# Performance work log

Hardware: AMD Instinct MI355X
Metric: run time of the kernel (lower is better)

The kernel has to match this reference:

```python
import jax, jax.numpy as jnp
import numpy as np

EPS = 1e-06  # used both as eps and as the F.threshold threshold (mqjs passes eps as th)


def _pair_log_dist_sum(x1, x2, th):
    # dist[i,j] = ||x1_i||^2 + ||x2_j||^2 - 2 x1_i . x2_j  (n x n)
    x1x2 = x1 @ x2.T
    sq1 = jnp.sum(x1 * x1, axis=1)[:, None]
    sq2 = jnp.sum(x2 * x2, axis=1)[None, :]
    dist = sq1 + sq2 - 2.0 * x1x2
    # F.threshold(dist, th, 1): values <= th -> 1; then clamp(min=1), sqrt, log, row-sum
    dist = jnp.where(dist > th, dist, 1.0)
    dist = jnp.maximum(dist, 1.0)
    return jnp.sum(0.5 * jnp.log(dist), axis=1)  # log(sqrt(d)) == 0.5*log(d)


def _mqjs(inp, tgt, eps):
    n = inp.shape[0]
    x1 = inp.reshape(n, -1)
    x2 = tgt.reshape(n, -1)
    p = (x1 + x2) / 2.0
    ce = _pair_log_dist_sum(x1, p, eps) + _pair_log_dist_sum(x2, p, eps)
    se = _pair_log_dist_sum(x1, x1, eps) * (n / (n - 1))
    return jnp.mean(ce - se)


def setup_inputs() -> dict:
    key = jax.random.key(0)
    k1, k2 = jax.random.split(key)
    n, d = 8192, 256
    inp = jax.random.normal(k1, (n, d), dtype=jnp.float32)
    tgt = jax.random.normal(k2, (n, d), dtype=jnp.float32)
    return {"input": inp, "target": tgt}


def reference(input, target):
    return _mqjs(input, target, EPS)
```

## Files before the change

kernel.cpp:

```cpp
#include <hip/hip_runtime.h>

#define N 8192
#define D 256
#define BM 128
#define BJ 64
#define JG 8
#define GJ (N / BJ / JG)
#define GI (N / BM)
#define NPART (3 * GI * GJ)

typedef int   i32x4 __attribute__((ext_vector_type(4)));
typedef int   i32x8 __attribute__((ext_vector_type(8)));
typedef float f32x4 __attribute__((ext_vector_type(4)));
typedef float f32x2 __attribute__((ext_vector_type(2)));

__device__ __forceinline__ unsigned pack_fp8x4(float a, float b, float c, float d) {
    unsigned lo = __builtin_amdgcn_cvt_pk_fp8_f32(a, b, 0, false);
    return __builtin_amdgcn_cvt_pk_fp8_f32(c, d, lo, true);
}
__device__ __forceinline__ float dequant_sumsq(unsigned q) {
    const float v0 = __builtin_amdgcn_cvt_f32_fp8(q, 0);
    const float v1 = __builtin_amdgcn_cvt_f32_fp8(q, 1);
    const float v2 = __builtin_amdgcn_cvt_f32_fp8(q, 2);
    const float v3 = __builtin_amdgcn_cvt_f32_fp8(q, 3);
    return fmaf(v0, v0, fmaf(v1, v1, fmaf(v2, v2, v3 * v3)));
}

__global__ void prep_kernel(const float* __restrict__ x1, const float* __restrict__ x2,
                            unsigned* __restrict__ x1q, unsigned* __restrict__ x2q,
                            unsigned* __restrict__ pq,
                            float* __restrict__ sq1, float* __restrict__ sq2,
                            float* __restrict__ sqp) {
    const int tid = threadIdx.x, lane = tid & 63, wv = tid >> 6;
    const int row = blockIdx.x * 4 + wv;
    const size_t eb = (size_t)row * D + lane * 4;
    const float4 a = *(const float4*)(x1 + eb);
    const float4 b = *(const float4*)(x2 + eb);
    const float px = 0.5f * (a.x + b.x), py = 0.5f * (a.y + b.y);
    const float pz = 0.5f * (a.z + b.z), pw = 0.5f * (a.w + b.w);
    const unsigned qa = pack_fp8x4(a.x, a.y, a.z, a.w);
    const unsigned qb = pack_fp8x4(b.x, b.y, b.z, b.w);
    const unsigned qp = pack_fp8x4(px, py, pz, pw);
    const size_t wb = (size_t)row * (D / 4) + lane;
    x1q[wb] = qa; x2q[wb] = qb; pq[wb] = qp;
    float s1 = dequant_sumsq(qa), s2 = dequant_sumsq(qb), sp = dequant_sumsq(qp);
    #pragma unroll
    for (int o = 32; o > 0; o >>= 1) {
        s1 += __shfl_down(s1, o, 64);
        s2 += __shfl_down(s2, o, 64);
        sp += __shfl_down(sp, o, 64);
    }
    if (lane == 0) { sq1[row] = s1; sq2[row] = s2; sqp[row] = sp; }
}

__device__ __forceinline__ f32x4 mfma8(i32x8 a, i32x8 b, f32x4 c) {
    return __builtin_amdgcn_mfma_scale_f32_16x16x128_f8f6f4(
        a, b, c, 0, 0, 0, 0x7F7F7F7F, 0, 0x7F7F7F7F);
}

__device__ __forceinline__ i32x8 read_frag(const unsigned char* Ts, int m, int quad) {
    const int r7 = m & 7;
    const i32x4 lo = *(const i32x4*)(Ts + m * 128 + ((((2 * quad)     ^ r7)) << 4));
    const i32x4 hi = *(const i32x4*)(Ts + m * 128 + ((((2 * quad + 1) ^ r7)) << 4));
    i32x8 f;
    f[0] = lo[0]; f[1] = lo[1]; f[2] = lo[2]; f[3] = lo[3];
    f[4] = hi[0]; f[5] = hi[1]; f[6] = hi[2]; f[7] = hi[3];
    return f;
}

__device__ __forceinline__ void stageB(const unsigned char* __restrict__ g,
                                       unsigned char* s, int rowbase, size_t kb,
                                       int wv, int srow, int sblk) {
    #pragma unroll
    for (int it = 0; it < 2; ++it) {
        const int grp = wv * 2 + it;
        const int row = grp * 8 + srow;
        __builtin_amdgcn_global_load_lds(
            (const __attribute__((address_space(1))) void*)(g + (size_t)(rowbase + row) * D + kb + sblk * 16),
            (__attribute__((address_space(3))) void*)(s + grp * 1024), 16, 0, 0);
    }
}

__device__ __forceinline__ float logsumP(const f32x4 (&acc)[4][2],
                                         const f32x2 (&sa01)[4], const f32x2 (&sa23)[4],
                                         const float sb[2]) {
    float s = 0.0f;
    #pragma unroll
    for (int ti = 0; ti < 4; ++ti) {
        f32x2 pr = {1.0f, 1.0f};
        #pragma unroll
        for (int tj = 0; tj < 2; ++tj) {
            const f32x2 sbv = {sb[tj], sb[tj]};
            const f32x2 t01 = sa01[ti] + sbv, t23 = sa23[ti] + sbv;
            const f32x2 v01 = {acc[ti][tj][0], acc[ti][tj][1]};
            const f32x2 v23 = {acc[ti][tj][2], acc[ti][tj][3]};
            f32x2 d01 = t01 - 2.0f * v01;
            f32x2 d23 = t23 - 2.0f * v23;
            d01 = __builtin_elementwise_max(d01, (f32x2){1.0f, 1.0f});
            d23 = __builtin_elementwise_max(d23, (f32x2){1.0f, 1.0f});
            pr *= d01; pr *= d23;
        }
        s += __logf(pr.x * pr.y);
    }
    return s;
}

__device__ __forceinline__ float logsumStraddle(const f32x4 (&acc)[4][2],
                                                const f32x2 (&sa01)[4], const f32x2 (&sa23)[4],
                                                const float sb[2],
                                                int wr, int wc, int quad, int l15,
                                                int I0, int J0) {
    float s = 0.0f;
    #pragma unroll
    for (int ti = 0; ti < 4; ++ti) {
        #pragma unroll
        for (int tj = 0; tj < 2; ++tj) {
            const int j = J0 + wc * 32 + tj * 16 + l15;
            float pr = 1.0f;
            #pragma unroll
            for (int r = 0; r < 4; ++r) {
                const int i = I0 + wr * 64 + ti * 16 + quad * 4 + r;
                const float sav = (r < 2) ? ((r & 1) ? sa01[ti].y : sa01[ti].x)
                                          : ((r & 1) ? sa23[ti].y : sa23[ti].x);
                float d = fmaf(-2.0f, acc[ti][tj][r], sav + sb[tj]);
                d = fmaxf(d, 1.0f);
                const float t = (j > i) ? d : 1.0f;
                const float u = (j >= i) ? d : 1.0f;
                pr *= t * u;
            }
            s += __logf(pr);
        }
    }
    return s;
}

__global__ __launch_bounds__(256) void mqjs_main(
    const unsigned char* __restrict__ x1q, const unsigned char* __restrict__ x2q,
    const unsigned char* __restrict__ pq,
    const float* __restrict__ sq1, const float* __restrict__ sq2,
    const float* __restrict__ sqp, float* __restrict__ partials) {

    __shared__ __align__(16) unsigned char Bs[2][2 * BJ * 128];
    __shared__ float red[4];

    const int tid = threadIdx.x;
    const int lane = tid & 63;
    const int wv = tid >> 6;
    const int wr = wv >> 1, wc = wv & 1;
    const int quad = lane >> 4, l15 = lane & 15;
    const int srow = lane >> 3;
    const int sblk = (lane & 7) ^ srow;

    const int z = blockIdx.z;
    const int I0 = blockIdx.y * BM;
    const int jbase = blockIdx.x * JG;
    const int pid = (z * GI + blockIdx.y) * GJ + blockIdx.x;
    const float wse = -(float)N / (float)(N - 1);

    int jj0 = 0;
    if (z == 2) {
        jj0 = 2 * (int)blockIdx.y - jbase;
        if (jj0 < 0) jj0 = 0;
        if (jj0 >= JG) { if (tid == 0) partials[pid] = 0.0f; return; }
    }

    const unsigned char* Ag = (z == 1) ? x2q : x1q;
    const unsigned char* Bg = (z == 2) ? x1q : pq;
    const float* sqAg = (z == 1) ? sq2 : sq1;
    const float* sqBg = (z == 2) ? sq1 : sqp;

    i32x8 af[2][4];
    f32x2 sa01[4], sa23[4];
    #pragma unroll
    for (int ti = 0; ti < 4; ++ti) {
        #pragma unroll
        for (int kc = 0; kc < 2; ++kc) {
            const size_t ro = (size_t)(I0 + wr * 64 + ti * 16 + l15) * D + kc * 128 + quad * 32;
            af[kc][ti] = *(const i32x8*)(Ag + ro);
        }
        const int sbase = I0 + wr * 64 + ti * 16 + quad * 4;
        sa01[ti] = (f32x2){sqAg[sbase], sqAg[sbase + 1]};
        sa23[ti] = (f32x2){sqAg[sbase + 2], sqAg[sbase + 3]};
    }

    stageB(Bg, Bs[0],        (jbase + jj0) * BJ, 0,   wv, srow, sblk);
    stageB(Bg, Bs[0] + 8192, (jbase + jj0) * BJ, 128, wv, srow, sblk);
    __syncthreads();

    float tsum = 0.0f;

    for (int jj = jj0; jj < JG; ++jj) {
        const int J0 = (jbase + jj) * BJ;
        const int buf = (jj - jj0) & 1;

        float sb[2];
        #pragma unroll
        for (int tj = 0; tj < 2; ++tj) sb[tj] = sqBg[J0 + wc * 32 + tj * 16 + l15];

        f32x4 acc[4][2];
        #pragma unroll
        for (int a = 0; a < 4; ++a)
            #pragma unroll
            for (int b = 0; b < 2; ++b)
                acc[a][b] = (f32x4){0.f, 0.f, 0.f, 0.f};
        #pragma unroll
        for (int kc = 0; kc < 2; ++kc) {
            i32x8 bfr[2];
            #pragma unroll
            for (int tj = 0; tj < 2; ++tj)
                bfr[tj] = read_frag(Bs[buf] + kc * 8192, wc * 32 + tj * 16 + l15, quad);
            #pragma unroll
            for (int ti = 0; ti < 4; ++ti)
                #pragma unroll
                for (int tj = 0; tj < 2; ++tj)
                    acc[ti][tj] = mfma8(af[kc][ti], bfr[tj], acc[ti][tj]);
        }

        if (jj < JG - 1) {
            stageB(Bg, Bs[buf ^ 1],        (jbase + jj + 1) * BJ, 0,   wv, srow, sblk);
            stageB(Bg, Bs[buf ^ 1] + 8192, (jbase + jj + 1) * BJ, 128, wv, srow, sblk);
        }

        if (z < 2) {
            tsum += 0.5f * logsumP(acc, sa01, sa23, sb);
        } else if (J0 >= I0 + BM) {
            tsum += wse * logsumP(acc, sa01, sa23, sb);
        } else {
            tsum += 0.5f * wse * logsumStraddle(acc, sa01, sa23, sb, wr, wc, quad, l15, I0, J0);
        }

        if (jj < JG - 1) __syncthreads();
    }

    #pragma unroll
    for (int o = 32; o > 0; o >>= 1) tsum += __shfl_down(tsum, o, 64);
    if (lane == 0) red[wv] = tsum;
    __syncthreads();
    if (tid == 0) partials[pid] = red[0] + red[1] + red[2] + red[3];
}

__global__ void finalize_kernel(const float* __restrict__ partials, float* __restrict__ out) {
    const int tid = threadIdx.x;
    const float4 v = ((const float4*)partials)[tid];
    double s = (double)v.x + (double)v.y + (double)v.z + (double)v.w;
    #pragma unroll
    for (int o = 32; o > 0; o >>= 1) s += __shfl_down(s, o, 64);
    __shared__ double r[12];
    if ((tid & 63) == 0) r[tid >> 6] = s;
    __syncthreads();
    if (tid == 0) {
        double t = 0.0;
        #pragma unroll
        for (int i = 0; i < 12; ++i) t += r[i];
        out[0] = (float)(t / (double)N);
    }
}

extern "C" void kernel_launch(void* const* d_in, const int* in_sizes, int n_in,
                              void* d_out, int out_size, void* d_ws, size_t ws_size,
                              hipStream_t stream) {
    const float* x1 = (const float*)d_in[0];
    const float* x2 = (const float*)d_in[1];

    char* ws = (char*)d_ws;
    const size_t MBYTES = (size_t)N * D;
    unsigned* x1q = (unsigned*)(ws);
    unsigned* x2q = (unsigned*)(ws + MBYTES);
    unsigned* pq  = (unsigned*)(ws + 2 * MBYTES);
    float* sq1 = (float*)(ws + 3 * MBYTES);
    float* sq2 = (float*)(ws + 3 * MBYTES + (size_t)N * 4);
    float* sqp = (float*)(ws + 3 * MBYTES + (size_t)N * 8);
    float* partials = (float*)(ws + 3 * MBYTES + (size_t)N * 12);

    prep_kernel<<<N / 4, 256, 0, stream>>>(x1, x2, x1q, x2q, pq, sq1, sq2, sqp);
    mqjs_main<<<dim3(GJ, GI, 3), 256, 0, stream>>>(
        (const unsigned char*)x1q, (const unsigned char*)x2q, (const unsigned char*)pq,
        sq1, sq2, sqp, partials);
    finalize_kernel<<<1, 768, 0, stream>>>(partials, (float*)d_out);
}
```

Measured before the change: 144.3 us.

## Load B fragments directly from global memory, dropping LDS staging and barriers

Removes the double-buffered LDS staging of the B tile (global_load_lds plus swizzled fragment reads) and has each wave load its B MFMA fragments straight from global memory into registers. This eliminates shared memory use and the per-iteration __syncthreads. In exchange, each B row is fetched separately by both wave rows with no explicit prefetch of the next tile, so more load traffic goes through L1/L2 and global latency may be exposed before the MFMAs.

```diff
diff --git a/kernel.cpp b/kernel.cpp
--- a/kernel.cpp
+++ b/kernel.cpp
@@ -9,7 +9,6 @@
 #define GI (N / BM)
 #define NPART (3 * GI * GJ)
 
-typedef int   i32x4 __attribute__((ext_vector_type(4)));
 typedef int   i32x8 __attribute__((ext_vector_type(8)));
 typedef float f32x4 __attribute__((ext_vector_type(4)));
 typedef float f32x2 __attribute__((ext_vector_type(2)));
@@ -58,29 +57,6 @@
         a, b, c, 0, 0, 0, 0x7F7F7F7F, 0, 0x7F7F7F7F);
 }
 
-__device__ __forceinline__ i32x8 read_frag(const unsigned char* Ts, int m, int quad) {
-    const int r7 = m & 7;
-    const i32x4 lo = *(const i32x4*)(Ts + m * 128 + ((((2 * quad)     ^ r7)) << 4));
-    const i32x4 hi = *(const i32x4*)(Ts + m * 128 + ((((2 * quad + 1) ^ r7)) << 4));
-    i32x8 f;
-    f[0] = lo[0]; f[1] = lo[1]; f[2] = lo[2]; f[3] = lo[3];
-    f[4] = hi[0]; f[5] = hi[1]; f[6] = hi[2]; f[7] = hi[3];
-    return f;
-}
-
-__device__ __forceinline__ void stageB(const unsigned char* __restrict__ g,
-                                       unsigned char* s, int rowbase, size_t kb,
-                                       int wv, int srow, int sblk) {
-    #pragma unroll
-    for (int it = 0; it < 2; ++it) {
-        const int grp = wv * 2 + it;
-        const int row = grp * 8 + srow;
-        __builtin_amdgcn_global_load_lds(
-            (const __attribute__((address_space(1))) void*)(g + (size_t)(rowbase + row) * D + kb + sblk * 16),
-            (__attribute__((address_space(3))) void*)(s + grp * 1024), 16, 0, 0);
-    }
-}
-
 __device__ __forceinline__ float logsumP(const f32x4 (&acc)[4][2],
                                          const f32x2 (&sa01)[4], const f32x2 (&sa23)[4],
                                          const float sb[2]) {
@@ -140,7 +116,6 @@
     const float* __restrict__ sq1, const float* __restrict__ sq2,
     const float* __restrict__ sqp, float* __restrict__ partials) {
 
-    __shared__ __align__(16) unsigned char Bs[2][2 * BJ * 128];
     __shared__ float red[4];
 
     const int tid = threadIdx.x;
@@ -148,8 +123,6 @@
     const int wv = tid >> 6;
     const int wr = wv >> 1, wc = wv & 1;
     const int quad = lane >> 4, l15 = lane & 15;
-    const int srow = lane >> 3;
-    const int sblk = (lane & 7) ^ srow;
 
     const int z = blockIdx.z;
     const int I0 = blockIdx.y * BM;
@@ -183,15 +156,18 @@
         sa23[ti] = (f32x2){sqAg[sbase + 2], sqAg[sbase + 3]};
     }
 
-    stageB(Bg, Bs[0],        (jbase + jj0) * BJ, 0,   wv, srow, sblk);
-    stageB(Bg, Bs[0] + 8192, (jbase + jj0) * BJ, 128, wv, srow, sblk);
-    __syncthreads();
-
     float tsum = 0.0f;
 
     for (int jj = jj0; jj < JG; ++jj) {
         const int J0 = (jbase + jj) * BJ;
-        const int buf = (jj - jj0) & 1;
+
+        i32x8 bfr[2][2];
+        #pragma unroll
+        for (int kc = 0; kc < 2; ++kc)
+            #pragma unroll
+            for (int tj = 0; tj < 2; ++tj)
+                bfr[kc][tj] = *(const i32x8*)(Bg +
+                    (size_t)(J0 + wc * 32 + tj * 16 + l15) * D + kc * 128 + quad * 32);
 
         float sb[2];
         #pragma unroll
@@ -204,22 +180,12 @@
             for (int b = 0; b < 2; ++b)
                 acc[a][b] = (f32x4){0.f, 0.f, 0.f, 0.f};
         #pragma unroll
-        for (int kc = 0; kc < 2; ++kc) {
-            i32x8 bfr[2];
-            #pragma unroll
-            for (int tj = 0; tj < 2; ++tj)
-                bfr[tj] = read_frag(Bs[buf] + kc * 8192, wc * 32 + tj * 16 + l15, quad);
+        for (int kc = 0; kc < 2; ++kc)
             #pragma unroll
             for (int ti = 0; ti < 4; ++ti)
                 #pragma unroll
                 for (int tj = 0; tj < 2; ++tj)
-                    acc[ti][tj] = mfma8(af[kc][ti], bfr[tj], acc[ti][tj]);
-        }
-
-        if (jj < JG - 1) {
-            stageB(Bg, Bs[buf ^ 1],        (jbase + jj + 1) * BJ, 0,   wv, srow, sblk);
-            stageB(Bg, Bs[buf ^ 1] + 8192, (jbase + jj + 1) * BJ, 128, wv, srow, sblk);
-        }
+                    acc[ti][tj] = mfma8(af[kc][ti], bfr[kc][tj], acc[ti][tj]);
 
         if (z < 2) {
             tsum += 0.5f * logsumP(acc, sa01, sa23, sb);
@@ -228,8 +194,6 @@
         } else {
             tsum += 0.5f * wse * logsumStraddle(acc, sa01, sa23, sb, wr, wc, quad, l15, I0, J0);
         }
-
-        if (jj < JG - 1) __syncthreads();
     }
 
     #pragma unroll
```

Measured after the change: 180.4 us. +25.1%, slower.
